# Performance work log

Hardware: AMD Instinct MI355X
Metric: run time of the kernel (lower is better)

The kernel has to match this reference:

```python
import jax, jax.numpy as jnp
import numpy as np

B, LQ, LK = 4, 2048, 2048
DIM = 1024          # intermediate_dim
H, D = 16, 64       # num_heads, head_dim
AD = H * D          # attn_dim
SCALE = 1.0 / np.sqrt(D).astype(np.float32)


def setup_inputs() -> dict:
    key = jax.random.key(0)
    ks = jax.random.split(key, 12)
    init = lambda k, shape, fan_in: jax.random.normal(k, shape, jnp.float32) / np.sqrt(fan_in).astype(np.float32)
    return {
        "x": jax.random.normal(ks[0], (B, LQ, DIM), jnp.float32),
        "embeds": jax.random.normal(ks[1], (B, LK, DIM), jnp.float32),
        "Wq": init(ks[2], (DIM, AD), DIM), "bq": jnp.zeros((AD,), jnp.float32),
        "Wk": init(ks[3], (DIM, AD), DIM), "bk": jnp.zeros((AD,), jnp.float32),
        "Wv": init(ks[4], (DIM, AD), DIM), "bv": jnp.zeros((AD,), jnp.float32),
        "Wo": init(ks[5], (AD, DIM), AD), "bo": jnp.zeros((DIM,), jnp.float32),
    }


def reference(x, embeds, Wq, bq, Wk, bk, Wv, bv, Wo, bo):
    b, lq, _ = x.shape
    lk = embeds.shape[1]
    # separate QKV projections (cross-attention: K,V from embeds)
    q = (x @ Wq + bq).reshape(b, lq, H, D)
    k = (embeds @ Wk + bk).reshape(b, lk, H, D)
    v = (embeds @ Wv + bv).reshape(b, lk, H, D)
    # scaled dot-product attention; full [b,h,lq,lk] score matrix (as in source)
    scores = jnp.einsum("bqhd,bkhd->bhqk", q, k) * SCALE
    attn = jax.nn.softmax(scores, axis=-1)  # dropout is identity at eval
    ctx = jnp.einsum("bhqk,bkhd->bqhd", attn, v).reshape(b, lq, AD)
    return ctx @ Wo + bo
```

## Files before the change

kernel.cpp:

```cpp
#include <hip/hip_runtime.h>
#include <cstdint>
#include <cstddef>

#define NB   4
#define NLQ  2048
#define NLK  2048
#define NDIM 1024
#define NH   16
#define ND   64
#define NAD  1024

typedef __attribute__((ext_vector_type(8))) short bf16x8;
typedef __attribute__((ext_vector_type(4))) short sh4;
typedef __attribute__((ext_vector_type(4))) float f32x4;
typedef __attribute__((ext_vector_type(4))) int   i32x4;

static __device__ __forceinline__ short f2bf(float f) {
    unsigned u = __builtin_bit_cast(unsigned, f);
    u += 0x7fffu + ((u >> 16) & 1u);
    return (short)(u >> 16);
}

#define GLL16(GP, LP) __builtin_amdgcn_global_load_lds( \
    (const __attribute__((address_space(1))) void*)(GP), \
    (__attribute__((address_space(3))) void*)(LP), 16, 0, 0)

#define SYNC_LDS do { \
    __builtin_amdgcn_sched_barrier(0); \
    asm volatile("s_waitcnt lgkmcnt(0)" ::: "memory"); \
    __builtin_amdgcn_s_barrier(); \
    asm volatile("" ::: "memory"); \
    __builtin_amdgcn_sched_barrier(0); } while (0)

__global__ void prep(const float* __restrict__ x, const float* __restrict__ e,
                     short* __restrict__ xo, short* __restrict__ eo,
                     const float* __restrict__ W0, const float* __restrict__ W1,
                     const float* __restrict__ W2, const float* __restrict__ W3,
                     short* __restrict__ T0, short* __restrict__ T1,
                     short* __restrict__ T2, short* __restrict__ T3) {
    __shared__ float t[32][33];
    const int id = blockIdx.x;
    if (id < 16384) {
        const float* in = (id >= 8192) ? e : x;
        short* out = (id >= 8192) ? eo : xo;
        const int i = ((id & 8191) * 256 + threadIdx.x) * 4;
        const float4 v = *(const float4*)(in + i);
        sh4 o;
        o.x = f2bf(v.x); o.y = f2bf(v.y); o.z = f2bf(v.z); o.w = f2bf(v.w);
        *(sh4*)(out + i) = o;
    } else {
        const int w = id - 16384;
        const int z = w >> 10;
        const int rem = w & 1023;
        const float* W = (z == 0) ? W0 : (z == 1) ? W1 : (z == 2) ? W2 : W3;
        short* Wt = (z == 0) ? T0 : (z == 1) ? T1 : (z == 2) ? T2 : T3;
        const int bx = (rem & 31) * 32;
        const int by = (rem >> 5) * 32;
        const int tx = threadIdx.x & 31, ty = threadIdx.x >> 5;
        #pragma unroll
        for (int i = 0; i < 32; i += 8)
            t[ty + i][tx] = W[(size_t)(bx + ty + i) * 1024 + by + tx];
        __syncthreads();
        #pragma unroll
        for (int i = 0; i < 32; i += 8)
            Wt[(size_t)(by + ty + i) * 1024 + bx + tx] = f2bf(t[tx][ty + i]);
    }
}

static __device__ __forceinline__ void xcd_tile_remap(int f, int& bx, int& by) {
    bx = ((f & 7) << 3) | ((f >> 3) & 7);
    by = f >> 6;
}


__global__ __launch_bounds__(256) void gemm_qkv(const short* __restrict__ Xb,
                                                const short* __restrict__ Eb,
                                                const short* __restrict__ Wqt,
                                                const short* __restrict__ Wkt,
                                                const short* __restrict__ Wvt,
                                                const float* __restrict__ bq,
                                                const float* __restrict__ bk,
                                                const float* __restrict__ bv,
                                                short* __restrict__ Qb,
                                                short* __restrict__ Kf,
                                                short* __restrict__ Vtb)
{
    const int N = 1024, K = 1024;
    __shared__ __align__(16) short As[128 * 64];
    __shared__ __align__(16) short Bs[128 * 64];
    const int z = blockIdx.z;
    const short* A    = (z == 0) ? Xb : Eb;
    const short* Wt   = (z == 0) ? Wqt : (z == 1) ? Wkt : Wvt;
    const float* bias = (z == 0) ? bq : (z == 1) ? bk : bv;
    const float scale = (z == 0) ? 0.18033688011112042f : 1.0f;

    const int tid = threadIdx.x, wave = tid >> 6, lane = tid & 63;
    const int quad = lane >> 4, col = lane & 15;
    int bx, by;
    xcd_tile_remap(blockIdx.x + (blockIdx.y << 6), bx, by);
    const int m0 = bx * 128, n0 = by * 128;
    const int wm = wave >> 1, wn = wave & 1;

    const f32x4 zero = {0.f, 0.f, 0.f, 0.f};
    f32x4 acc[4][4];
    #pragma unroll
    for (int i = 0; i < 4; ++i)
        #pragma unroll
        for (int j = 0; j < 4; ++j)
            acc[i][j] = zero;

    for (int kt = 0; kt < K / 64; ++kt) {
        __syncthreads();
        #pragma unroll
        for (int i = 0; i < 4; ++i) {
            const int f = (i * 4 + wave) * 512 + lane * 8;
            const int row = f >> 6, ch = (f >> 3) & 7;
            const int gcol = kt * 64 + ((ch ^ (row & 7)) * 8);
            GLL16(A  + (size_t)(m0 + row) * K + gcol, &As[f]);
            GLL16(Wt + (size_t)(n0 + row) * K + gcol, &Bs[f]);
        }
        __syncthreads();
        #pragma unroll
        for (int kk = 0; kk < 2; ++kk) {
            bf16x8 af[4], bfr[4];
            #pragma unroll
            for (int mt = 0; mt < 4; ++mt) {
                const int r = wm * 64 + mt * 16 + col;
                af[mt] = *(const bf16x8*)&As[r * 64 + (((kk * 4 + quad) ^ (r & 7)) * 8)];
            }
            #pragma unroll
            for (int nt = 0; nt < 4; ++nt) {
                const int r = wn * 64 + nt * 16 + col;
                bfr[nt] = *(const bf16x8*)&Bs[r * 64 + (((kk * 4 + quad) ^ (r & 7)) * 8)];
            }
            #pragma unroll
            for (int mt = 0; mt < 4; ++mt)
                #pragma unroll
                for (int nt = 0; nt < 4; ++nt)
                    acc[mt][nt] = __builtin_amdgcn_mfma_f32_16x16x32_bf16(af[mt], bfr[nt], acc[mt][nt], 0, 0, 0);
        }
    }

    if (z < 2) {
        short* outp = (z == 0) ? Qb : Kf;
        #pragma unroll
        for (int mt = 0; mt < 4; ++mt)
            #pragma unroll
            for (int nt = 0; nt < 4; ++nt) {
                const int n = n0 + wn * 64 + nt * 16 + col;
                const float bv_ = bias[n];
                #pragma unroll
                for (int r = 0; r < 4; ++r) {
                    const int m = m0 + wm * 64 + mt * 16 + quad * 4 + r;
                    outp[(size_t)m * N + n] = f2bf((acc[mt][nt][r] + bv_) * scale);
                }
            }
    } else {
        #pragma unroll
        for (int mt = 0; mt < 4; ++mt)
            #pragma unroll
            for (int nt = 0; nt < 4; ++nt) {
                const int n = n0 + wn * 64 + nt * 16 + col;
                const int hh = n >> 6, d = n & 63;
                const float bv_ = bias[n];
                const int mb = m0 + wm * 64 + mt * 16 + quad * 4;
                const int bb = mb >> 11, s = mb & 2047;
                sh4 o4;
                #pragma unroll
                for (int r = 0; r < 4; ++r)
                    o4[r] = f2bf(acc[mt][nt][r] + bv_);
                *(sh4*)&Vtb[((size_t)((bb * NH + hh) * 64 + d)) * NLK + s] = o4;
            }
    }
}

__global__ __launch_bounds__(256) void gemm_out(const short* __restrict__ A,
                                                const short* __restrict__ Wt,
                                                const float* __restrict__ bias,
                                                float* __restrict__ outp)
{
    const int N = 1024, K = 1024;
    __shared__ __align__(16) short As[128 * 64];
    __shared__ __align__(16) short Bs[128 * 64];
    const int tid = threadIdx.x, wave = tid >> 6, lane = tid & 63;
    const int quad = lane >> 4, col = lane & 15;
    int bx, by;
    xcd_tile_remap(blockIdx.x + (blockIdx.y << 6), bx, by);
    const int m0 = bx * 128, n0 = by * 128;
    const int wm = wave >> 1, wn = wave & 1;

    const f32x4 zero = {0.f, 0.f, 0.f, 0.f};
    f32x4 acc[4][4];
    #pragma unroll
    for (int i = 0; i < 4; ++i)
        #pragma unroll
        for (int j = 0; j < 4; ++j)
            acc[i][j] = zero;

    for (int kt = 0; kt < K / 64; ++kt) {
        __syncthreads();
        #pragma unroll
        for (int i = 0; i < 4; ++i) {
            const int f = (i * 4 + wave) * 512 + lane * 8;
            const int row = f >> 6, ch = (f >> 3) & 7;
            const int gcol = kt * 64 + ((ch ^ (row & 7)) * 8);
            GLL16(A  + (size_t)(m0 + row) * K + gcol, &As[f]);
            GLL16(Wt + (size_t)(n0 + row) * K + gcol, &Bs[f]);
        }
        __syncthreads();
        #pragma unroll
        for (int kk = 0; kk < 2; ++kk) {
            bf16x8 af[4], bfr[4];
            #pragma unroll
            for (int mt = 0; mt < 4; ++mt) {
                const int r = wm * 64 + mt * 16 + col;
                af[mt] = *(const bf16x8*)&As[r * 64 + (((kk * 4 + quad) ^ (r & 7)) * 8)];
            }
            #pragma unroll
            for (int nt = 0; nt < 4; ++nt) {
                const int r = wn * 64 + nt * 16 + col;
                bfr[nt] = *(const bf16x8*)&Bs[r * 64 + (((kk * 4 + quad) ^ (r & 7)) * 8)];
            }
            #pragma unroll
            for (int mt = 0; mt < 4; ++mt)
                #pragma unroll
                for (int nt = 0; nt < 4; ++nt)
                    acc[mt][nt] = __builtin_amdgcn_mfma_f32_16x16x32_bf16(af[mt], bfr[nt], acc[mt][nt], 0, 0, 0);
        }
    }

    #pragma unroll
    for (int mt = 0; mt < 4; ++mt)
        #pragma unroll
        for (int nt = 0; nt < 4; ++nt) {
            const int n = n0 + wn * 64 + nt * 16 + col;
            const float bv_ = bias[n];
            #pragma unroll
            for (int r = 0; r < 4; ++r) {
                const int m = m0 + wm * 64 + mt * 16 + quad * 4 + r;
                outp[(size_t)m * N + n] = acc[mt][nt][r] + bv_;
            }
        }
}

__global__ __launch_bounds__(256, 2) void attn_fused12(const short* __restrict__ Q,
                                                       const short* __restrict__ Kb,
                                                       const short* __restrict__ Vt,
                                                       short* __restrict__ ctx)
{
    __shared__ __align__(16) short Ks[2][64 * 64];
    __shared__ __align__(16) short Vs[2][64 * 64];
    const int tid = threadIdx.x, wave = tid >> 6, lane = tid & 63;
    const int quad = lane >> 4, col = lane & 15;

    const int p = blockIdx.x;
    const int g = ((p >> 3) & 7) * 8 + (p & 7);
    const int qt = p >> 6;
    const int h = g & 15, b = g >> 4;
    const int q0 = qt * 256 + wave * 64;

    bf16x8 aq[4][2];
    #pragma unroll
    for (int mt = 0; mt < 4; ++mt) {
        const short* qp = Q + (size_t)(b * NLQ + q0 + mt * 16 + col) * NAD + h * 64 + quad * 8;
        aq[mt][0] = *(const bf16x8*)qp;
        aq[mt][1] = *(const bf16x8*)(qp + 32);
    }

    bf16x8 vones;
    #pragma unroll
    for (int j = 0; j < 8; ++j) vones[j] = (short)0x3F80;

    const f32x4 zero = {0.f, 0.f, 0.f, 0.f};
    f32x4 O[4][4];
    f32x4 Ol[4];
    #pragma unroll
    for (int mt = 0; mt < 4; ++mt) {
        Ol[mt] = zero;
        #pragma unroll
        for (int db = 0; db < 4; ++db) O[db][mt] = zero;
    }

    const int srow = tid >> 3, schunk = tid & 7;
    const short* kbase = Kb + (size_t)b * NLK * NAD + h * 64 + schunk * 8;
    const short* vbase = Vt + (size_t)(b * NH + h) * 64 * NLK + schunk * 8;

    const int vt_ = schunk >> 2, vh_ = (schunk >> 1) & 1, vq0 = (schunk * 2) & 3;
    const int vcl = vt_ * 4 + vq0;
    const int voff = vh_ * 4;

    bf16x8 kv[2], vv[2];
    #pragma unroll
    for (int i = 0; i < 2; ++i) {
        const int row = i * 32 + srow;
        kv[i] = *(const bf16x8*)(kbase + (size_t)row * NAD);
        vv[i] = *(const bf16x8*)(vbase + (size_t)row * NLK);
    }

    for (int kt = 0; kt < NLK / 64; ++kt) {
        short* Kw = &Ks[kt & 1][0];
        short* Vw = &Vs[kt & 1][0];
        #pragma unroll
        for (int i = 0; i < 2; ++i) {
            const int row = i * 32 + srow;
            const int c = (schunk ^ (row & 7)) * 8;
            *(bf16x8*)&Kw[row * 64 + c] = kv[i];
            const sh4 lo = { vv[i][0], vv[i][1], vv[i][2], vv[i][3] };
            const sh4 hi = { vv[i][4], vv[i][5], vv[i][6], vv[i][7] };
            *(sh4*)&Vw[row * 64 + ((vcl ^ (row & 7)) * 8 + voff)] = lo;
            *(sh4*)&Vw[row * 64 + (((vcl + 1) ^ (row & 7)) * 8 + voff)] = hi;
        }

        const int nk = (kt + 1) & (NLK / 64 - 1);
        #pragma unroll
        for (int i = 0; i < 2; ++i) {
            const int row = i * 32 + srow;
            kv[i] = *(const bf16x8*)(kbase + (size_t)(nk * 64 + row) * NAD);
            vv[i] = *(const bf16x8*)(vbase + (size_t)row * NLK + nk * 64);
        }

        SYNC_LDS;

        bf16x8 kf[2][4];
        #pragma unroll
        for (int kk = 0; kk < 2; ++kk)
            #pragma unroll
            for (int nt = 0; nt < 4; ++nt) {
                const int key = nt * 16 + col;
                kf[kk][nt] = *(const bf16x8*)&Kw[key * 64 + (((kk * 4 + quad) ^ (key & 7)) * 8)];
            }

        int pk[4][2][4];
        #pragma unroll
        for (int mt = 0; mt < 4; ++mt) {
            f32x4 st[4];
            #pragma unroll
            for (int nt = 0; nt < 4; ++nt) st[nt] = zero;
            __builtin_amdgcn_s_setprio(1);
            #pragma unroll
            for (int kk = 0; kk < 2; ++kk)
                #pragma unroll
                for (int nt = 0; nt < 4; ++nt)
                    st[nt] = __builtin_amdgcn_mfma_f32_16x16x32_bf16(kf[kk][nt], aq[mt][kk], st[nt], 0, 0, 0);
            __builtin_amdgcn_s_setprio(0);
            #pragma unroll
            for (int nt = 0; nt < 4; ++nt) {
                const unsigned u0 = __builtin_bit_cast(unsigned, __builtin_amdgcn_exp2f(st[nt][0]));
                const unsigned u1 = __builtin_bit_cast(unsigned, __builtin_amdgcn_exp2f(st[nt][1]));
                const unsigned u2 = __builtin_bit_cast(unsigned, __builtin_amdgcn_exp2f(st[nt][2]));
                const unsigned u3 = __builtin_bit_cast(unsigned, __builtin_amdgcn_exp2f(st[nt][3]));
                const int t = nt >> 1, odd = (nt & 1) * 2;
                pk[mt][t][odd + 0] = (int)__builtin_amdgcn_perm(u1, u0, 0x07060302u);
                pk[mt][t][odd + 1] = (int)__builtin_amdgcn_perm(u3, u2, 0x07060302u);
            }
            __builtin_amdgcn_s_setprio(1);
            #pragma unroll
            for (int t = 0; t < 2; ++t) {
                const bf16x8 pb = __builtin_bit_cast(bf16x8,
                    i32x4{pk[mt][t][0], pk[mt][t][1], pk[mt][t][2], pk[mt][t][3]});
                Ol[mt] = __builtin_amdgcn_mfma_f32_16x16x32_bf16(vones, pb, Ol[mt], 0, 0, 0);
            }
            __builtin_amdgcn_s_setprio(0);
        }

        #pragma unroll
        for (int t = 0; t < 2; ++t)
            #pragma unroll
            for (int db = 0; db < 4; ++db) {
                const int row = db * 16 + col;
                const bf16x8 va = *(const bf16x8*)&Vw[row * 64 + (((t * 4 + quad) ^ (row & 7)) * 8)];
                __builtin_amdgcn_s_setprio(1);
                #pragma unroll
                for (int mt = 0; mt < 4; ++mt) {
                    const bf16x8 pb = __builtin_bit_cast(bf16x8,
                        i32x4{pk[mt][t][0], pk[mt][t][1], pk[mt][t][2], pk[mt][t][3]});
                    O[db][mt] = __builtin_amdgcn_mfma_f32_16x16x32_bf16(va, pb, O[db][mt], 0, 0, 0);
                }
                __builtin_amdgcn_s_setprio(0);
            }
    }

    #pragma unroll
    for (int mt = 0; mt < 4; ++mt) {
        const float linv = 1.0f / Ol[mt][0];
        #pragma unroll
        for (int db = 0; db < 4; ++db) {
            sh4 o4;
            #pragma unroll
            for (int r = 0; r < 4; ++r)
                o4[r] = f2bf(O[db][mt][r] * linv);
            short* cp = ctx + (size_t)(b * NLQ + q0 + mt * 16 + col) * NAD
                      + h * 64 + db * 16 + quad * 4;
            *(sh4*)cp = o4;
        }
    }
}

extern "C" void kernel_launch(void* const* d_in, const int* in_sizes, int n_in,
                              void* d_out, int out_size, void* d_ws, size_t ws_size,
                              hipStream_t stream)
{
    (void)in_sizes; (void)n_in; (void)out_size; (void)ws_size;
    const float* x  = (const float*)d_in[0];
    const float* e  = (const float*)d_in[1];
    const float* Wq = (const float*)d_in[2];
    const float* bq = (const float*)d_in[3];
    const float* Wk = (const float*)d_in[4];
    const float* bk = (const float*)d_in[5];
    const float* Wv = (const float*)d_in[6];
    const float* bv = (const float*)d_in[7];
    const float* Wo = (const float*)d_in[8];
    const float* bo = (const float*)d_in[9];
    float* out = (float*)d_out;

    const size_t MQ = (size_t)NB * NLQ;
    short* wsp = (short*)d_ws;
    short* Xb  = wsp;
    short* Eb  = Xb  + MQ * NDIM;
    short* Wqt = Eb  + MQ * NDIM;
    short* Wkt = Wqt + (size_t)NDIM * NAD;
    short* Wvt = Wkt + (size_t)NDIM * NAD;
    short* Wot = Wvt + (size_t)NDIM * NAD;
    short* Qb  = Wot + (size_t)NDIM * NAD;
    short* Kf  = Qb  + MQ * NAD;
    short* Vtb = Kf  + MQ * NAD;
    short* Cx  = Vtb + MQ * NAD;

    prep<<<dim3(20480), 256, 0, stream>>>(x, e, Xb, Eb,
                                          Wq, Wk, Wv, Wo, Wqt, Wkt, Wvt, Wot);

    gemm_qkv<<<dim3(64, 8, 3), 256, 0, stream>>>(Xb, Eb, Wqt, Wkt, Wvt,
                                                 bq, bk, bv, Qb, Kf, Vtb);

    attn_fused12<<<dim3(NB * NH * (NLQ / 256)), 256, 0, stream>>>(Qb, Kf, Vtb, Cx);

    gemm_out<<<dim3(64, 8), 256, 0, stream>>>(Cx, Wot, bo, out);
}
```

Before: 286.7 us.

## Fuse attention and output projection into one kernel with a global barrier

Measured after the change: 342.1 us. 1.19x slower.

```diff
diff --git a/kernel.cpp b/kernel.cpp
--- a/kernel.cpp
+++ b/kernel.cpp
@@ -37,9 +37,11 @@
                      const float* __restrict__ W0, const float* __restrict__ W1,
                      const float* __restrict__ W2, const float* __restrict__ W3,
                      short* __restrict__ T0, short* __restrict__ T1,
-                     short* __restrict__ T2, short* __restrict__ T3) {
+                     short* __restrict__ T2, short* __restrict__ T3,
+                     unsigned* __restrict__ ctr) {
     __shared__ float t[32][33];
     const int id = blockIdx.x;
+    if (id == 0 && threadIdx.x == 0) *ctr = 0u;
     if (id < 16384) {
         const float* in = (id >= 8192) ? e : x;
         short* out = (id >= 8192) ? eo : xo;
@@ -71,7 +73,6 @@
     bx = ((f & 7) << 3) | ((f >> 3) & 7);
     by = f >> 6;
 }
-
 
 __global__ __launch_bounds__(256) void gemm_qkv(const short* __restrict__ Xb,
                                                 const short* __restrict__ Eb,
@@ -174,225 +175,236 @@
     }
 }
 
-__global__ __launch_bounds__(256) void gemm_out(const short* __restrict__ A,
-                                                const short* __restrict__ Wt,
-                                                const float* __restrict__ bias,
-                                                float* __restrict__ outp)
+__global__ __launch_bounds__(256, 2) void attn_out(const short* __restrict__ Q,
+                                                   const short* __restrict__ Kb,
+                                                   const short* __restrict__ Vt,
+                                                   const short* __restrict__ Wot,
+                                                   const float* __restrict__ bo,
+                                                   short* __restrict__ ctx,
+                                                   float* __restrict__ outp,
+                                                   unsigned* __restrict__ ctr)
 {
-    const int N = 1024, K = 1024;
-    __shared__ __align__(16) short As[128 * 64];
-    __shared__ __align__(16) short Bs[128 * 64];
+    __shared__ __align__(16) short smem[16384];
     const int tid = threadIdx.x, wave = tid >> 6, lane = tid & 63;
     const int quad = lane >> 4, col = lane & 15;
-    int bx, by;
-    xcd_tile_remap(blockIdx.x + (blockIdx.y << 6), bx, by);
-    const int m0 = bx * 128, n0 = by * 128;
-    const int wm = wave >> 1, wn = wave & 1;
-
-    const f32x4 zero = {0.f, 0.f, 0.f, 0.f};
-    f32x4 acc[4][4];
-    #pragma unroll
-    for (int i = 0; i < 4; ++i)
-        #pragma unroll
-        for (int j = 0; j < 4; ++j)
-            acc[i][j] = zero;
-
-    for (int kt = 0; kt < K / 64; ++kt) {
-        __syncthreads();
-        #pragma unroll
-        for (int i = 0; i < 4; ++i) {
-            const int f = (i * 4 + wave) * 512 + lane * 8;
-            const int row = f >> 6, ch = (f >> 3) & 7;
-            const int gcol = kt * 64 + ((ch ^ (row & 7)) * 8);
-            GLL16(A  + (size_t)(m0 + row) * K + gcol, &As[f]);
-            GLL16(Wt + (size_t)(n0 + row) * K + gcol, &Bs[f]);
-        }
-        __syncthreads();
-        #pragma unroll
-        for (int kk = 0; kk < 2; ++kk) {
-            bf16x8 af[4], bfr[4];
-            #pragma unroll
-            for (int mt = 0; mt < 4; ++mt) {
-                const int r = wm * 64 + mt * 16 + col;
-                af[mt] = *(const bf16x8*)&As[r * 64 + (((kk * 4 + quad) ^ (r & 7)) * 8)];
-            }
-            #pragma unroll
-            for (int nt = 0; nt < 4; ++nt) {
-                const int r = wn * 64 + nt * 16 + col;
-                bfr[nt] = *(const bf16x8*)&Bs[r * 64 + (((kk * 4 + quad) ^ (r & 7)) * 8)];
-            }
-            #pragma unroll
-            for (int mt = 0; mt < 4; ++mt)
-                #pragma unroll
-                for (int nt = 0; nt < 4; ++nt)
-                    acc[mt][nt] = __builtin_amdgcn_mfma_f32_16x16x32_bf16(af[mt], bfr[nt], acc[mt][nt], 0, 0, 0);
-        }
-    }
-
-    #pragma unroll
-    for (int mt = 0; mt < 4; ++mt)
-        #pragma unroll
-        for (int nt = 0; nt < 4; ++nt) {
-            const int n = n0 + wn * 64 + nt * 16 + col;
-            const float bv_ = bias[n];
-            #pragma unroll
-            for (int r = 0; r < 4; ++r) {
-                const int m = m0 + wm * 64 + mt * 16 + quad * 4 + r;
-                outp[(size_t)m * N + n] = acc[mt][nt][r] + bv_;
-            }
-        }
-}
-
-__global__ __launch_bounds__(256, 2) void attn_fused12(const short* __restrict__ Q,
-                                                       const short* __restrict__ Kb,
-                                                       const short* __restrict__ Vt,
-                                                       short* __restrict__ ctx)
-{
-    __shared__ __align__(16) short Ks[2][64 * 64];
-    __shared__ __align__(16) short Vs[2][64 * 64];
-    const int tid = threadIdx.x, wave = tid >> 6, lane = tid & 63;
-    const int quad = lane >> 4, col = lane & 15;
-
-    const int p = blockIdx.x;
-    const int g = ((p >> 3) & 7) * 8 + (p & 7);
-    const int qt = p >> 6;
-    const int h = g & 15, b = g >> 4;
-    const int q0 = qt * 256 + wave * 64;
-
-    bf16x8 aq[4][2];
-    #pragma unroll
-    for (int mt = 0; mt < 4; ++mt) {
-        const short* qp = Q + (size_t)(b * NLQ + q0 + mt * 16 + col) * NAD + h * 64 + quad * 8;
-        aq[mt][0] = *(const bf16x8*)qp;
-        aq[mt][1] = *(const bf16x8*)(qp + 32);
-    }
-
-    bf16x8 vones;
-    #pragma unroll
-    for (int j = 0; j < 8; ++j) vones[j] = (short)0x3F80;
-
-    const f32x4 zero = {0.f, 0.f, 0.f, 0.f};
-    f32x4 O[4][4];
-    f32x4 Ol[4];
-    #pragma unroll
-    for (int mt = 0; mt < 4; ++mt) {
-        Ol[mt] = zero;
-        #pragma unroll
-        for (int db = 0; db < 4; ++db) O[db][mt] = zero;
-    }
-
-    const int srow = tid >> 3, schunk = tid & 7;
-    const short* kbase = Kb + (size_t)b * NLK * NAD + h * 64 + schunk * 8;
-    const short* vbase = Vt + (size_t)(b * NH + h) * 64 * NLK + schunk * 8;
-
-    const int vt_ = schunk >> 2, vh_ = (schunk >> 1) & 1, vq0 = (schunk * 2) & 3;
-    const int vcl = vt_ * 4 + vq0;
-    const int voff = vh_ * 4;
-
-    bf16x8 kv[2], vv[2];
-    #pragma unroll
-    for (int i = 0; i < 2; ++i) {
-        const int row = i * 32 + srow;
-        kv[i] = *(const bf16x8*)(kbase + (size_t)row * NAD);
-        vv[i] = *(const bf16x8*)(vbase + (size_t)row * NLK);
-    }
-
-    for (int kt = 0; kt < NLK / 64; ++kt) {
-        short* Kw = &Ks[kt & 1][0];
-        short* Vw = &Vs[kt & 1][0];
+
+    {
+        short* KsB = smem;
+        short* VsB = smem + 8192;
+
+        const int p = blockIdx.x;
+        const int g = ((p >> 3) & 7) * 8 + (p & 7);
+        const int qt = p >> 6;
+        const int h = g & 15, b = g >> 4;
+        const int q0 = qt * 256 + wave * 64;
+
+        bf16x8 aq[4][2];
+        #pragma unroll
+        for (int mt = 0; mt < 4; ++mt) {
+            const short* qp = Q + (size_t)(b * NLQ + q0 + mt * 16 + col) * NAD + h * 64 + quad * 8;
+            aq[mt][0] = *(const bf16x8*)qp;
+            aq[mt][1] = *(const bf16x8*)(qp + 32);
+        }
+
+        bf16x8 vones;
+        #pragma unroll
+        for (int j = 0; j < 8; ++j) vones[j] = (short)0x3F80;
+
+        const f32x4 zero = {0.f, 0.f, 0.f, 0.f};
+        f32x4 O[4][4];
+        f32x4 Ol[4];
+        #pragma unroll
+        for (int mt = 0; mt < 4; ++mt) {
+            Ol[mt] = zero;
+            #pragma unroll
+            for (int db = 0; db < 4; ++db) O[db][mt] = zero;
+        }
+
+        const int srow = tid >> 3, schunk = tid & 7;
+        const short* kbase = Kb + (size_t)b * NLK * NAD + h * 64 + schunk * 8;
+        const short* vbase = Vt + (size_t)(b * NH + h) * 64 * NLK + schunk * 8;
+
+        const int vt_ = schunk >> 2, vh_ = (schunk >> 1) & 1, vq0 = (schunk * 2) & 3;
+        const int vcl = vt_ * 4 + vq0;
+        const int voff = vh_ * 4;
+
+        bf16x8 kv[2], vv[2];
         #pragma unroll
         for (int i = 0; i < 2; ++i) {
             const int row = i * 32 + srow;
-            const int c = (schunk ^ (row & 7)) * 8;
-            *(bf16x8*)&Kw[row * 64 + c] = kv[i];
-            const sh4 lo = { vv[i][0], vv[i][1], vv[i][2], vv[i][3] };
-            const sh4 hi = { vv[i][4], vv[i][5], vv[i][6], vv[i][7] };
-            *(sh4*)&Vw[row * 64 + ((vcl ^ (row & 7)) * 8 + voff)] = lo;
-            *(sh4*)&Vw[row * 64 + (((vcl + 1) ^ (row & 7)) * 8 + voff)] = hi;
-        }
-
-        const int nk = (kt + 1) & (NLK / 64 - 1);
-        #pragma unroll
-        for (int i = 0; i < 2; ++i) {
-            const int row = i * 32 + srow;
-            kv[i] = *(const bf16x8*)(kbase + (size_t)(nk * 64 + row) * NAD);
-            vv[i] = *(const bf16x8*)(vbase + (size_t)row * NLK + nk * 64);
-        }
-
-        SYNC_LDS;
-
-        bf16x8 kf[2][4];
-        #pragma unroll
-        for (int kk = 0; kk < 2; ++kk)
-            #pragma unroll
-            for (int nt = 0; nt < 4; ++nt) {
-                const int key = nt * 16 + col;
-                kf[kk][nt] = *(const bf16x8*)&Kw[key * 64 + (((kk * 4 + quad) ^ (key & 7)) * 8)];
-            }
-
-        int pk[4][2][4];
-        #pragma unroll
-        for (int mt = 0; mt < 4; ++mt) {
-            f32x4 st[4];
-            #pragma unroll
-            for (int nt = 0; nt < 4; ++nt) st[nt] = zero;
-            __builtin_amdgcn_s_setprio(1);
+            kv[i] = *(const bf16x8*)(kbase + (size_t)row * NAD);
+            vv[i] = *(const bf16x8*)(vbase + (size_t)row * NLK);
+        }
+
+        for (int kt = 0; kt < NLK / 64; ++kt) {
+            short* Kw = KsB + (kt & 1) * 4096;
+            short* Vw = VsB + (kt & 1) * 4096;
+            #pragma unroll
+            for (int i = 0; i < 2; ++i) {
+                const int row = i * 32 + srow;
+                const int c = (schunk ^ (row & 7)) * 8;
+                *(bf16x8*)&Kw[row * 64 + c] = kv[i];
+                const sh4 lo = { vv[i][0], vv[i][1], vv[i][2], vv[i][3] };
+                const sh4 hi = { vv[i][4], vv[i][5], vv[i][6], vv[i][7] };
+                *(sh4*)&Vw[row * 64 + ((vcl ^ (row & 7)) * 8 + voff)] = lo;
+                *(sh4*)&Vw[row * 64 + (((vcl + 1) ^ (row & 7)) * 8 + voff)] = hi;
+            }
+
+            const int nk = (kt + 1) & (NLK / 64 - 1);
+            #pragma unroll
+            for (int i = 0; i < 2; ++i) {
+                const int row = i * 32 + srow;
+                kv[i] = *(const bf16x8*)(kbase + (size_t)(nk * 64 + row) * NAD);
+                vv[i] = *(const bf16x8*)(vbase + (size_t)row * NLK + nk * 64);
+            }
+
+            SYNC_LDS;
+
+            bf16x8 kf[2][4];
             #pragma unroll
             for (int kk = 0; kk < 2; ++kk)
                 #pragma unroll
-                for (int nt = 0; nt < 4; ++nt)
-                    st[nt] = __builtin_amdgcn_mfma_f32_16x16x32_bf16(kf[kk][nt], aq[mt][kk], st[nt], 0, 0, 0);
-            __builtin_amdgcn_s_setprio(0);
-            #pragma unroll
-            for (int nt = 0; nt < 4; ++nt) {
-                const unsigned u0 = __builtin_bit_cast(unsigned, __builtin_amdgcn_exp2f(st[nt][0]));
-                const unsigned u1 = __builtin_bit_cast(unsigned, __builtin_amdgcn_exp2f(st[nt][1]));
-                const unsigned u2 = __builtin_bit_cast(unsigned, __builtin_amdgcn_exp2f(st[nt][2]));
-                const unsigned u3 = __builtin_bit_cast(unsigned, __builtin_amdgcn_exp2f(st[nt][3]));
-                const int t = nt >> 1, odd = (nt & 1) * 2;
-                pk[mt][t][odd + 0] = (int)__builtin_amdgcn_perm(u1, u0, 0x07060302u);
-                pk[mt][t][odd + 1] = (int)__builtin_amdgcn_perm(u3, u2, 0x07060302u);
-            }
-            __builtin_amdgcn_s_setprio(1);
-            #pragma unroll
-            for (int t = 0; t < 2; ++t) {
-                const bf16x8 pb = __builtin_bit_cast(bf16x8,
-                    i32x4{pk[mt][t][0], pk[mt][t][1], pk[mt][t][2], pk[mt][t][3]});
-                Ol[mt] = __builtin_amdgcn_mfma_f32_16x16x32_bf16(vones, pb, Ol[mt], 0, 0, 0);
-            }
-            __builtin_amdgcn_s_setprio(0);
-        }
-
-        #pragma unroll
-        for (int t = 0; t < 2; ++t)
-            #pragma unroll
-            for (int db = 0; db < 4; ++db) {
-                const int row = db * 16 + col;
-                const bf16x8 va = *(const bf16x8*)&Vw[row * 64 + (((t * 4 + quad) ^ (row & 7)) * 8)];
+                for (int nt = 0; nt < 4; ++nt) {
+                    const int key = nt * 16 + col;
+                    kf[kk][nt] = *(const bf16x8*)&Kw[key * 64 + (((kk * 4 + quad) ^ (key & 7)) * 8)];
+                }
+
+            int pk[4][2][4];
+            #pragma unroll
+            for (int mt = 0; mt < 4; ++mt) {
+                f32x4 st[4];
+                #pragma unroll
+                for (int nt = 0; nt < 4; ++nt) st[nt] = zero;
                 __builtin_amdgcn_s_setprio(1);
                 #pragma unroll
-                for (int mt = 0; mt < 4; ++mt) {
+                for (int kk = 0; kk < 2; ++kk)
+                    #pragma unroll
+                    for (int nt = 0; nt < 4; ++nt)
+                        st[nt] = __builtin_amdgcn_mfma_f32_16x16x32_bf16(kf[kk][nt], aq[mt][kk], st[nt], 0, 0, 0);
+                __builtin_amdgcn_s_setprio(0);
+                #pragma unroll
+                for (int nt = 0; nt < 4; ++nt) {
+                    const unsigned u0 = __builtin_bit_cast(unsigned, __builtin_amdgcn_exp2f(st[nt][0]));
+                    const unsigned u1 = __builtin_bit_cast(unsigned, __builtin_amdgcn_exp2f(st[nt][1]));
+                    const unsigned u2 = __builtin_bit_cast(unsigned, __builtin_amdgcn_exp2f(st[nt][2]));
+                    const unsigned u3 = __builtin_bit_cast(unsigned, __builtin_amdgcn_exp2f(st[nt][3]));
+                    const int t = nt >> 1, odd = (nt & 1) * 2;
+                    pk[mt][t][odd + 0] = (int)__builtin_amdgcn_perm(u1, u0, 0x07060302u);
+                    pk[mt][t][odd + 1] = (int)__builtin_amdgcn_perm(u3, u2, 0x07060302u);
+                }
+                __builtin_amdgcn_s_setprio(1);
+                #pragma unroll
+                for (int t = 0; t < 2; ++t) {
                     const bf16x8 pb = __builtin_bit_cast(bf16x8,
                         i32x4{pk[mt][t][0], pk[mt][t][1], pk[mt][t][2], pk[mt][t][3]});
-                    O[db][mt] = __builtin_amdgcn_mfma_f32_16x16x32_bf16(va, pb, O[db][mt], 0, 0, 0);
+                    Ol[mt] = __builtin_amdgcn_mfma_f32_16x16x32_bf16(vones, pb, Ol[mt], 0, 0, 0);
                 }
                 __builtin_amdgcn_s_setprio(0);
             }
-    }
-
-    #pragma unroll
-    for (int mt = 0; mt < 4; ++mt) {
-        const float linv = 1.0f / Ol[mt][0];
-        #pragma unroll
-        for (int db = 0; db < 4; ++db) {
-            sh4 o4;
-            #pragma unroll
-            for (int r = 0; r < 4; ++r)
-                o4[r] = f2bf(O[db][mt][r] * linv);
-            short* cp = ctx + (size_t)(b * NLQ + q0 + mt * 16 + col) * NAD
-                      + h * 64 + db * 16 + quad * 4;
-            *(sh4*)cp = o4;
-        }
+
+            #pragma unroll
+            for (int t = 0; t < 2; ++t)
+                #pragma unroll
+                for (int db = 0; db < 4; ++db) {
+                    const int row = db * 16 + col;
+                    const bf16x8 va = *(const bf16x8*)&Vw[row * 64 + (((t * 4 + quad) ^ (row & 7)) * 8)];
+                    __builtin_amdgcn_s_setprio(1);
+                    #pragma unroll
+                    for (int mt = 0; mt < 4; ++mt) {
+                        const bf16x8 pb = __builtin_bit_cast(bf16x8,
+                            i32x4{pk[mt][t][0], pk[mt][t][1], pk[mt][t][2], pk[mt][t][3]});
+                        O[db][mt] = __builtin_amdgcn_mfma_f32_16x16x32_bf16(va, pb, O[db][mt], 0, 0, 0);
+                    }
+                    __builtin_amdgcn_s_setprio(0);
+                }
+        }
+
+        #pragma unroll
+        for (int mt = 0; mt < 4; ++mt) {
+            const float linv = 1.0f / Ol[mt][0];
+            #pragma unroll
+            for (int db = 0; db < 4; ++db) {
+                sh4 o4;
+                #pragma unroll
+                for (int r = 0; r < 4; ++r)
+                    o4[r] = f2bf(O[db][mt][r] * linv);
+                short* cp = ctx + (size_t)(b * NLQ + q0 + mt * 16 + col) * NAD
+                          + h * 64 + db * 16 + quad * 4;
+                *(sh4*)cp = o4;
+            }
+        }
+    }
+
+    __syncthreads();
+    if (tid == 0) {
+        __threadfence();
+        atomicAdd(ctr, 1u);
+        while (atomicAdd(ctr, 0u) < 512u) __builtin_amdgcn_s_sleep(8);
+        __threadfence();
+    }
+    __syncthreads();
+
+    {
+        const int N = 1024, K = 1024;
+        short* As = smem;
+        short* Bs = smem + 8192;
+        int bx, by;
+        xcd_tile_remap(blockIdx.x, bx, by);
+        const int m0 = bx * 128, n0 = by * 128;
+        const int wm = wave >> 1, wn = wave & 1;
+
+        const f32x4 zero = {0.f, 0.f, 0.f, 0.f};
+        f32x4 acc[4][4];
+        #pragma unroll
+        for (int i = 0; i < 4; ++i)
+            #pragma unroll
+            for (int j = 0; j < 4; ++j)
+                acc[i][j] = zero;
+
+        for (int kt = 0; kt < K / 64; ++kt) {
+            __syncthreads();
+            #pragma unroll
+            for (int i = 0; i < 4; ++i) {
+                const int f = (i * 4 + wave) * 512 + lane * 8;
+                const int row = f >> 6, ch = (f >> 3) & 7;
+                const int gcol = kt * 64 + ((ch ^ (row & 7)) * 8);
+                GLL16(ctx + (size_t)(m0 + row) * K + gcol, &As[f]);
+                GLL16(Wot + (size_t)(n0 + row) * K + gcol, &Bs[f]);
+            }
+            __syncthreads();
+            #pragma unroll
+            for (int kk = 0; kk < 2; ++kk) {
+                bf16x8 af[4], bfr[4];
+                #pragma unroll
+                for (int mt = 0; mt < 4; ++mt) {
+                    const int r = wm * 64 + mt * 16 + col;
+                    af[mt] = *(const bf16x8*)&As[r * 64 + (((kk * 4 + quad) ^ (r & 7)) * 8)];
+                }
+                #pragma unroll
+                for (int nt = 0; nt < 4; ++nt) {
+                    const int r = wn * 64 + nt * 16 + col;
+                    bfr[nt] = *(const bf16x8*)&Bs[r * 64 + (((kk * 4 + quad) ^ (r & 7)) * 8)];
+                }
+                #pragma unroll
+                for (int mt = 0; mt < 4; ++mt)
+                    #pragma unroll
+                    for (int nt = 0; nt < 4; ++nt)
+                        acc[mt][nt] = __builtin_amdgcn_mfma_f32_16x16x32_bf16(af[mt], bfr[nt], acc[mt][nt], 0, 0, 0);
+            }
+        }
+
+        #pragma unroll
+        for (int mt = 0; mt < 4; ++mt)
+            #pragma unroll
+            for (int nt = 0; nt < 4; ++nt) {
+                const int n = n0 + wn * 64 + nt * 16 + col;
+                const float bv_ = bo[n];
+                #pragma unroll
+                for (int r = 0; r < 4; ++r) {
+                    const int m = m0 + wm * 64 + mt * 16 + quad * 4 + r;
+                    outp[(size_t)m * N + n] = acc[mt][nt][r] + bv_;
+                }
+            }
     }
 }
 
@@ -425,14 +437,13 @@
     short* Kf  = Qb  + MQ * NAD;
     short* Vtb = Kf  + MQ * NAD;
     short* Cx  = Vtb + MQ * NAD;
+    unsigned* ctr = (unsigned*)(Cx + MQ * NAD);
 
     prep<<<dim3(20480), 256, 0, stream>>>(x, e, Xb, Eb,
-                                          Wq, Wk, Wv, Wo, Wqt, Wkt, Wvt, Wot);
+                                          Wq, Wk, Wv, Wo, Wqt, Wkt, Wvt, Wot, ctr);
 
     gemm_qkv<<<dim3(64, 8, 3), 256, 0, stream>>>(Xb, Eb, Wqt, Wkt, Wvt,
                                                  bq, bk, bv, Qb, Kf, Vtb);
 
-    attn_fused12<<<dim3(NB * NH * (NLQ / 256)), 256, 0, stream>>>(Qb, Kf, Vtb, Cx);
-
-    gemm_out<<<dim3(64, 8), 256, 0, stream>>>(Cx, Wot, bo, out);
-}
+    attn_out<<<dim3(512), 256, 0, stream>>>(Qb, Kf, Vtb, Wot, bo, Cx, out, ctr);
+}
```
